# Kernel optimization log

Hardware: AMD Instinct MI355X
Metric: run time of the kernel (lower is better)

Reference implementation:

```python
import jax, jax.numpy as jnp
import numpy as np

V = 50000
E = 800000
D_IN = 128
D_OUT = 128
NUM_REL = 200
BN_EPS = 1e-5


def setup_inputs() -> dict:
    key = jax.random.key(0)
    ks = jax.random.split(key, 12)
    return {
        "x": jax.random.normal(ks[0], (V, D_IN), dtype=jnp.float32),
        "rel_repr": jax.random.normal(ks[1], (NUM_REL, D_IN), dtype=jnp.float32),
        "edge_norm": jax.random.uniform(ks[2], (E,), dtype=jnp.float32),
        "in_w": jax.random.normal(ks[3], (D_IN, D_OUT), dtype=jnp.float32) * 0.1,
        "out_w": jax.random.normal(ks[4], (D_IN, D_OUT), dtype=jnp.float32) * 0.1,
        "loop_w": jax.random.normal(ks[5], (D_IN, D_OUT), dtype=jnp.float32) * 0.1,
        "w_rel": jax.random.normal(ks[6], (D_IN, D_OUT), dtype=jnp.float32) * 0.1,
        "loop_rel": jax.random.normal(ks[7], (1, D_IN), dtype=jnp.float32),
        "bias": jnp.zeros((D_OUT,), dtype=jnp.float32),
        "bn_gamma": jnp.ones((D_OUT,), dtype=jnp.float32),
        "bn_beta": jnp.zeros((D_OUT,), dtype=jnp.float32),
        "edge_type": jax.random.randint(ks[8], (E,), 0, NUM_REL, dtype=jnp.int32),
        "src": jax.random.randint(ks[9], (E,), 0, V, dtype=jnp.int32),
        "dst": jax.random.randint(ks[10], (E,), 0, V, dtype=jnp.int32),
    }


def reference(x, rel_repr, edge_norm, in_w, out_w, loop_w, w_rel, loop_rel,
              bias, bn_gamma, bn_beta, edge_type, src, dst):
    # rel_wt is None (num_base=-1) -> rel = rel_repr directly
    rel = rel_repr

    # message: comp='mult' composition of gathered src features and relation emb
    edge_data = x[src] * rel[edge_type]                      # [E, D_IN]
    half = edge_data.shape[0] // 2
    # first half of edges through in_w, second half through out_w (CompGCN convention)
    msg = jnp.concatenate(
        [edge_data[:half] @ in_w, edge_data[half:] @ out_w], axis=0
    ) * edge_norm[:, None]                                   # [E, D_OUT]

    # agg='sum': scatter-reduce into destination nodes (zero for isolated nodes)
    h_agg = jax.ops.segment_sum(msg, dst, num_segments=V)    # [V, D_OUT]

    # self-loop branch: comp(x, loop_rel) @ loop_w, comb='add', scaled by 1/3
    loop = (x * loop_rel) @ loop_w                           # [V, D_OUT]
    h = (h_agg + loop) * (1.0 / 3.0)

    h = h + bias

    # BatchNorm1d (training mode: batch statistics over node dim)
    mean = jnp.mean(h, axis=0)
    var = jnp.var(h, axis=0)
    h = (h - mean) * jax.lax.rsqrt(var + BN_EPS) * bn_gamma + bn_beta

    out_x = jax.nn.relu(h)                                   # act='relu'
    out_rel = rel @ w_rel                                    # ltr=True
    return (out_x, out_rel)
```

## Files before the change

kernel.cpp:

```cpp
#include <hip/hip_runtime.h>
#include <hip/hip_bf16.h>


#define SCAN_BLOCK 256
#define CB 128
#define CHUNK 4096
#define NBC_MAX 800
#define CAP 3072
#define RED1 64
#define NGB 128

typedef __attribute__((ext_vector_type(8))) short short8v;
typedef __attribute__((ext_vector_type(4))) float float4v;

__device__ inline short f2bf(float f) {
    union { float f; unsigned u; } c; c.f = f;
    unsigned u = c.u;
    return (short)((u + 0x7fffu + ((u >> 16) & 1u)) >> 16);
}
__device__ inline unsigned packbf(float a, float b) {
    return (unsigned)(unsigned short)f2bf(a) |
           ((unsigned)(unsigned short)f2bf(b) << 16);
}
__device__ inline float bflo(unsigned u) { return __uint_as_float(u << 16); }
__device__ inline float bfhi(unsigned u) { return __uint_as_float(u & 0xffff0000u); }

__global__ __launch_bounds__(256) void xcast_kernel(
    const float* __restrict__ x, const float* __restrict__ rel,
    short* __restrict__ xbf, short* __restrict__ relbf, int V, int R)
{
    size_t i = ((size_t)blockIdx.x * 256 + threadIdx.x) * 8;
    size_t nx = (size_t)V * 128;
    size_t total = nx + (size_t)R * 128;
    if (i >= total) return;
    const float* sp; short* dp; size_t k;
    if (i < nx) { sp = x; dp = xbf; k = i; }
    else        { sp = rel; dp = relbf; k = i - nx; }
    float4 v0 = *reinterpret_cast<const float4*>(sp + k);
    float4 v1 = *reinterpret_cast<const float4*>(sp + k + 4);
    short8v o;
    o[0] = f2bf(v0.x); o[1] = f2bf(v0.y); o[2] = f2bf(v0.z); o[3] = f2bf(v0.w);
    o[4] = f2bf(v1.x); o[5] = f2bf(v1.y); o[6] = f2bf(v1.z); o[7] = f2bf(v1.w);
    *reinterpret_cast<short8v*>(dp + k) = o;
}

__global__ __launch_bounds__(256) void hist_coarse_kernel(
    const int* __restrict__ dst, int* __restrict__ counts,
    int E, int V, int NBC)
{
    __shared__ int lh[NBC_MAX];
    for (int i = threadIdx.x; i < NBC; i += 256) lh[i] = 0;
    __syncthreads();
    int half = E >> 1;
    int e0 = blockIdx.x * CHUNK;
    for (int i = 0; i < CHUNK / 256; ++i) {
        int e = e0 + i * 256 + threadIdx.x;
        if (e < E) {
            int key = dst[e] + (e < half ? 0 : V);
            atomicAdd(&lh[key >> 7], 1);
        }
    }
    __syncthreads();
    for (int i = threadIdx.x; i < NBC; i += 256)
        counts[(size_t)blockIdx.x * NBC + i] = lh[i];
}

__global__ __launch_bounds__(SCAN_BLOCK) void scan_partial_t_kernel(
    const int* __restrict__ cnt_bm, int* __restrict__ partials,
    int CN, int NBC, int NBLK)
{
    __shared__ int red[SCAN_BLOCK];
    int l = blockIdx.x * SCAN_BLOCK + threadIdx.x;
    int v = 0;
    if (l < CN) {
        int bu = l / NBLK, bl = l - bu * NBLK;
        v = cnt_bm[(size_t)bl * NBC + bu];
    }
    red[threadIdx.x] = v;
    __syncthreads();
    for (int s = SCAN_BLOCK / 2; s > 0; s >>= 1) {
        if (threadIdx.x < s) red[threadIdx.x] += red[threadIdx.x + s];
        __syncthreads();
    }
    if (threadIdx.x == 0) partials[blockIdx.x] = red[0];
}

__global__ __launch_bounds__(1024) void scan_top_kernel(
    int* __restrict__ partials, int NB)
{
    __shared__ int sh[1024];
    int t = threadIdx.x;
    sh[t] = (t < NB) ? partials[t] : 0;
    __syncthreads();
    for (int s = 1; s < 1024; s <<= 1) {
        int v = (t >= s) ? sh[t - s] : 0;
        __syncthreads();
        sh[t] += v;
        __syncthreads();
    }
    if (t < NB) partials[t] = (t == 0) ? 0 : sh[t - 1];
}

__global__ __launch_bounds__(SCAN_BLOCK) void scan_final_t_kernel(
    const int* __restrict__ cnt_bm, const int* __restrict__ partials,
    int* __restrict__ base, int CN, int NBC, int NBLK)
{
    __shared__ int sh[SCAN_BLOCK];
    int l = blockIdx.x * SCAN_BLOCK + threadIdx.x;
    int t = threadIdx.x;
    int v = 0;
    if (l < CN) {
        int bu = l / NBLK, bl = l - bu * NBLK;
        v = cnt_bm[(size_t)bl * NBC + bu];
    }
    sh[t] = v;
    __syncthreads();
    for (int s = 1; s < SCAN_BLOCK; s <<= 1) {
        int u = (t >= s) ? sh[t - s] : 0;
        __syncthreads();
        sh[t] += u;
        __syncthreads();
    }
    if (l < CN) base[l] = partials[blockIdx.x] + sh[t] - v;
}

__global__ __launch_bounds__(256) void rank_coarse_kernel(
    const int* __restrict__ dst,
    const int* __restrict__ src,
    const int* __restrict__ edge_type,
    const float* __restrict__ edge_norm,
    const int* __restrict__ base,
    uint2* __restrict__ pay,
    int E, int V, int NBC, int NBLK)
{
    __shared__ int lh[NBC_MAX];
    __shared__ int lb[NBC_MAX];
    for (int i = threadIdx.x; i < NBC; i += 256) {
        lh[i] = 0;
        lb[i] = base[(size_t)i * NBLK + blockIdx.x];
    }
    __syncthreads();
    int half = E >> 1;
    int e0 = blockIdx.x * CHUNK;
    for (int i = 0; i < CHUNK / 256; ++i) {
        int e = e0 + i * 256 + threadIdx.x;
        if (e < E) {
            int d = dst[e], s = src[e], t = edge_type[e];
            float n = edge_norm[e];
            int key = d + (e < half ? 0 : V);
            int b = key >> 7;
            int r = atomicAdd(&lh[b], 1);
            pay[lb[b] + r] = make_uint2(
                ((unsigned)s << 16) | ((unsigned)t << 8) | (unsigned)(key & 127),
                __float_as_uint(n));
        }
    }
}

__global__ __launch_bounds__(256) void fine_sort_kernel(
    const uint2* __restrict__ pay,
    const int* __restrict__ base,
    uint2* __restrict__ pay2,
    int* __restrict__ foffg,
    int E, int NK, int NBC, int NBLK)
{
    __shared__ uint2 pay_s[CAP];
    __shared__ int fcnt[CB];
    __shared__ int ssc[CB];
    __shared__ int fcur[CB];

    int b = blockIdx.x;
    int beg = base[(size_t)b * NBLK];
    int end = (b + 1 < NBC) ? base[(size_t)(b + 1) * NBLK] : E;
    int cnt = end - beg;
    int tid = threadIdx.x;

    if (tid < CB) fcnt[tid] = 0;
    __syncthreads();
    for (int j = tid; j < cnt; j += 256)
        atomicAdd(&fcnt[pay[beg + j].x & 127u], 1);
    __syncthreads();
    if (tid < CB) ssc[tid] = fcnt[tid];
    __syncthreads();
    for (int s = 1; s < CB; s <<= 1) {
        int v = 0;
        if (tid < CB && tid >= s) v = ssc[tid - s];
        __syncthreads();
        if (tid < CB) ssc[tid] += v;
        __syncthreads();
    }
    if (tid < CB) {
        int ex = ssc[tid] - fcnt[tid];
        fcur[tid] = ex;
        int key = b * CB + tid;
        if (key <= NK) foffg[key] = beg + ex;
    }
    __syncthreads();

    if (cnt <= CAP) {
        for (int j = tid; j < cnt; j += 256) {
            uint2 p = pay[beg + j];
            int r = atomicAdd(&fcur[p.x & 127u], 1);
            pay_s[r] = p;
        }
        __syncthreads();
        for (int j = tid; j < cnt; j += 256) pay2[beg + j] = pay_s[j];
    } else {
        for (int j = tid; j < cnt; j += 256) {
            uint2 p = pay[beg + j];
            int r = atomicAdd(&fcur[p.x & 127u], 1);
            pay2[beg + r] = p;
        }
    }
}

__global__ __launch_bounds__(256) void aggregate_g16_kernel(
    const short* __restrict__ xbf,
    const short* __restrict__ relbf,
    const uint2* __restrict__ pay2,
    const int* __restrict__ foffg,
    short* __restrict__ accbf,
    int NK, int E)
{
    int wid = (blockIdx.x * 256 + threadIdx.x) >> 6;
    int lane = threadIdx.x & 63;
    int g = lane >> 4;
    int sub = lane & 15;
    int k = wid * 4 + g;
    if (k >= NK) k = NK - 1;
    int f0 = sub << 3;

    int beg = foffg[k];
    int end = foffg[k + 1];
    int cnt = end - beg;

    int maxc = cnt;
    maxc = max(maxc, __shfl_xor(maxc, 16, 64));
    maxc = max(maxc, __shfl_xor(maxc, 32, 64));

    float a0 = 0.f, a1 = 0.f, a2 = 0.f, a3 = 0.f;
    float a4 = 0.f, a5 = 0.f, a6 = 0.f, a7 = 0.f;

    for (int bas = 0; bas < maxc; bas += 16) {
        int off = bas + sub;
        int cidx = (cnt > 0) ? min(off, cnt - 1) : 0;
        int j = min(beg + cidx, E - 1);
        uint2 p = pay2[j];
        int qmax = min(16, maxc - bas);
        for (int q = 0; q < qmax; ++q) {
            int srcl = (lane & 48) + q;
            unsigned pqx = __shfl(p.x, srcl, 64);
            unsigned pqn = __shfl(p.y, srcl, 64);
            float n = ((bas + q) < cnt) ? __uint_as_float(pqn) : 0.f;
            int s = (int)(pqx >> 16);
            int t = (int)((pqx >> 8) & 0xffu);
            uint4 xv = *reinterpret_cast<const uint4*>(xbf + (size_t)s * 128 + f0);
            uint4 rv = *reinterpret_cast<const uint4*>(relbf + (size_t)t * 128 + f0);
            a0 += bflo(xv.x) * bflo(rv.x) * n;
            a1 += bfhi(xv.x) * bfhi(rv.x) * n;
            a2 += bflo(xv.y) * bflo(rv.y) * n;
            a3 += bfhi(xv.y) * bfhi(rv.y) * n;
            a4 += bflo(xv.z) * bflo(rv.z) * n;
            a5 += bfhi(xv.z) * bfhi(rv.z) * n;
            a6 += bflo(xv.w) * bflo(rv.w) * n;
            a7 += bfhi(xv.w) * bfhi(rv.w) * n;
        }
    }
    uint4 o;
    o.x = packbf(a0, a1);
    o.y = packbf(a2, a3);
    o.z = packbf(a4, a5);
    o.w = packbf(a6, a7);
    *reinterpret_cast<uint4*>(accbf + (size_t)k * 128 + f0) = o;
}

__global__ __launch_bounds__(256) void wpack_kernel(
    const float* __restrict__ in_w,
    const float* __restrict__ out_w,
    const float* __restrict__ loop_w,
    const float* __restrict__ loop_rel,
    short* __restrict__ wpack)
{
    int idx = blockIdx.x * 256 + threadIdx.x;
    if (idx >= 3 * 8 * 4 * 64) return;
    int lane = idx & 63;
    int t    = (idx >> 6) & 3;
    int cblk = (idx >> 8) & 7;
    int m    = idx >> 11;
    const float* W = (m == 0) ? in_w : (m == 1) ? out_w : loop_w;
    int col = cblk * 16 + (lane & 15);
    int kb  = t * 32 + ((lane >> 4) << 3);
    short8v v;
#pragma unroll
    for (int j = 0; j < 8; ++j) {
        float w = W[(kb + j) * 128 + col];
        if (m == 2) w *= loop_rel[kb + j];
        v[j] = f2bf(w);
    }
    *reinterpret_cast<short8v*>(wpack + (size_t)idx * 8) = v;
}

__global__ __launch_bounds__(512) void fused_gemm_mfma_kernel(
    const short* __restrict__ accbf,
    const short* __restrict__ xbf,
    const short* __restrict__ wpack,
    const float* __restrict__ bias,
    short* __restrict__ hbf,
    float* __restrict__ stats_part,
    int V, int NRB)
{
    __shared__ short wlds[3 * 4 * 4 * 64 * 8];
    __shared__ float s_red[128];

    int tid  = threadIdx.x;
    int wave = tid >> 6;
    int lane = tid & 63;
    int kgrp = lane >> 4;
    int r16  = lane & 15;
    int bid  = blockIdx.x >> 1;
    int hh   = blockIdx.x & 1;

    if (tid < 128) s_red[tid] = 0.f;

    {
        const short8v* wsv = reinterpret_cast<const short8v*>(wpack);
        short8v* wldv = reinterpret_cast<short8v*>(wlds);
#pragma unroll
        for (int i = 0; i < 6; ++i) {
            int idx = i * 512 + tid;
            int l  = idx & 63;
            int t  = (idx >> 6) & 3;
            int cb = (idx >> 8) & 3;
            int m  = idx >> 10;
            wldv[idx] = wsv[(((size_t)m * 8 + (4 * hh + cb)) * 4 + t) * 64 + l];
        }
    }
    __syncthreads();

    const short8v* wldv = reinterpret_cast<const short8v*>(wlds);
    float ps[4] = {0.f, 0.f, 0.f, 0.f};
    float pq[4] = {0.f, 0.f, 0.f, 0.f};

    for (int rt = bid; rt < NRB; rt += NGB) {
        int row0 = rt * 128 + wave * 16;
        int rowl = row0 + r16;
        int rowc = min(rowl, V - 1);

        short8v af[3][4];
        {
            const short* A0 = accbf + (size_t)rowc * 128;
            const short* A1 = accbf + (size_t)(V + rowc) * 128;
            const short* A2 = xbf + (size_t)rowc * 128;
#pragma unroll
            for (int t = 0; t < 4; ++t) {
                int o = t * 32 + (kgrp << 3);
                af[0][t] = *reinterpret_cast<const short8v*>(A0 + o);
                af[1][t] = *reinterpret_cast<const short8v*>(A1 + o);
                af[2][t] = *reinterpret_cast<const short8v*>(A2 + o);
            }
        }

        float4v c[4];
#pragma unroll
        for (int b = 0; b < 4; ++b) c[b] = (float4v)(0.f);

#pragma unroll
        for (int m = 0; m < 3; ++m)
#pragma unroll
            for (int t = 0; t < 4; ++t) {
#pragma unroll
                for (int b = 0; b < 4; ++b) {
                    short8v bf_ = wldv[(((m * 4 + b) * 4) + t) * 64 + lane];
                    c[b] = __builtin_amdgcn_mfma_f32_16x16x32_bf16(af[m][t], bf_, c[b], 0, 0, 0);
                }
            }

#pragma unroll
        for (int b = 0; b < 4; ++b) {
            int col = hh * 64 + b * 16 + r16;
            float bv = bias[col];
#pragma unroll
            for (int r = 0; r < 4; ++r) {
                int row = row0 + kgrp * 4 + r;
                if (row < V) {
                    float v = c[b][r] * (1.f / 3.f) + bv;
                    hbf[(size_t)row * 128 + col] = f2bf(v);
                    ps[b] += v;
                    pq[b] += v * v;
                }
            }
        }
    }

#pragma unroll
    for (int b = 0; b < 4; ++b) {
        int cl = b * 16 + r16;
        atomicAdd(&s_red[cl], ps[b]);
        atomicAdd(&s_red[64 + cl], pq[b]);
    }
    __syncthreads();
    if (tid < 64)
        stats_part[(size_t)bid * 256 + hh * 64 + tid] = s_red[tid];
    else if (tid < 128)
        stats_part[(size_t)bid * 256 + 128 + hh * 64 + (tid - 64)] = s_red[tid];
}

__global__ __launch_bounds__(256) void bn_reduce1_kernel(
    const float* __restrict__ stats_part, float* __restrict__ stage, int NB)
{
    int col = threadIdx.x;
    float s = 0.f;
    for (int i = blockIdx.x; i < NB; i += RED1)
        s += stats_part[(size_t)i * 256 + col];
    stage[(size_t)blockIdx.x * 256 + col] = s;
}

__global__ __launch_bounds__(256) void bn_reduce2_kernel(
    const float* __restrict__ stage, float* __restrict__ stats)
{
    int col = threadIdx.x;
    float s0 = 0.f, s1 = 0.f, s2 = 0.f, s3 = 0.f;
#pragma unroll
    for (int i = 0; i < RED1; i += 4) {
        s0 += stage[(size_t)(i + 0) * 256 + col];
        s1 += stage[(size_t)(i + 1) * 256 + col];
        s2 += stage[(size_t)(i + 2) * 256 + col];
        s3 += stage[(size_t)(i + 3) * 256 + col];
    }
    stats[col] = (s0 + s1) + (s2 + s3);
}

__global__ __launch_bounds__(256) void bn_apply_kernel(
    const short* __restrict__ hbf,
    float* __restrict__ hout,
    const float* __restrict__ stats,
    const float* __restrict__ gamma,
    const float* __restrict__ beta,
    int V)
{
    int c4   = (threadIdx.x & 31) << 2;
    int rsub = threadIdx.x >> 5;
    float inv_v = 1.f / (float)V;
    float sc[4], sh[4];
#pragma unroll
    for (int j = 0; j < 4; ++j) {
        int col = c4 + j;
        float mean = stats[col] * inv_v;
        float var  = stats[128 + col] * inv_v - mean * mean;
        float s = rsqrtf(var + 1e-5f) * gamma[col];
        sc[j] = s;
        sh[j] = beta[col] - mean * s;
    }
    for (int row = blockIdx.x * 8 + rsub; row < V; row += gridDim.x * 8) {
        uint2 u = *reinterpret_cast<const uint2*>(hbf + (size_t)row * 128 + c4);
        float4 v;
        v.x = fmaxf(bflo(u.x) * sc[0] + sh[0], 0.f);
        v.y = fmaxf(bfhi(u.x) * sc[1] + sh[1], 0.f);
        v.z = fmaxf(bflo(u.y) * sc[2] + sh[2], 0.f);
        v.w = fmaxf(bfhi(u.y) * sc[3] + sh[3], 0.f);
        *reinterpret_cast<float4*>(hout + (size_t)row * 128 + c4) = v;
    }
}

__global__ __launch_bounds__(256) void rel_gemm_kernel(
    const float* __restrict__ rel,
    const float* __restrict__ w_rel,
    float* __restrict__ out_rel,
    int R)
{
    int col = threadIdx.x & 127;
    int row = blockIdx.x * 2 + (threadIdx.x >> 7);
    if (row >= R) return;
    float acc = 0.f;
    for (int k = 0; k < 128; ++k)
        acc += rel[row * 128 + k] * w_rel[k * 128 + col];
    out_rel[row * 128 + col] = acc;
}

extern "C" void kernel_launch(void* const* d_in, const int* in_sizes, int n_in,
                              void* d_out, int out_size, void* d_ws, size_t ws_size,
                              hipStream_t stream)
{
    const float* x         = (const float*)d_in[0];
    const float* rel_repr  = (const float*)d_in[1];
    const float* edge_norm = (const float*)d_in[2];
    const float* in_w      = (const float*)d_in[3];
    const float* out_w     = (const float*)d_in[4];
    const float* loop_w    = (const float*)d_in[5];
    const float* w_rel     = (const float*)d_in[6];
    const float* loop_rel  = (const float*)d_in[7];
    const float* bias      = (const float*)d_in[8];
    const float* bn_gamma  = (const float*)d_in[9];
    const float* bn_beta   = (const float*)d_in[10];
    const int* edge_type   = (const int*)d_in[11];
    const int* src         = (const int*)d_in[12];
    const int* dst         = (const int*)d_in[13];

    const int V = in_sizes[0] / 128;
    const int E = in_sizes[2];
    const int R = in_sizes[1] / 128;
    const int NK = 2 * V;
    const int NBC = (NK + CB - 1) / CB;
    const int NBLK = (E + CHUNK - 1) / CHUNK;
    const int CN = NBC * NBLK;
    const int NB2 = (CN + SCAN_BLOCK - 1) / SCAN_BLOCK;
    const int NRB = (V + 127) / 128;

    float* hout    = (float*)d_out;
    float* out_rel = hout + (size_t)V * 128;

    char* wp_ = (char*)d_ws;
    short* accbf    = (short*)wp_;  wp_ += (size_t)NK * 128 * sizeof(short);
    short* xbf      = (short*)wp_;  wp_ += (size_t)V * 128 * sizeof(short);
    short* relbf    = (short*)wp_;  wp_ += (size_t)R * 128 * sizeof(short);
    short* hbf      = (short*)wp_;  wp_ += (size_t)V * 128 * sizeof(short);
    short* wpack    = (short*)wp_;  wp_ += (size_t)3 * 8 * 4 * 64 * 8 * sizeof(short);
    float* stats    = (float*)wp_;  wp_ += 256 * sizeof(float);
    float* stats_pt = (float*)wp_;  wp_ += (size_t)NGB * 256 * sizeof(float);
    float* stage    = (float*)wp_;  wp_ += (size_t)RED1 * 256 * sizeof(float);
    int*   counts   = (int*)wp_;    wp_ += (size_t)CN * sizeof(int);
    int*   basep    = (int*)wp_;    wp_ += (size_t)CN * sizeof(int);
    int*   partials = (int*)wp_;    wp_ += 1024 * sizeof(int);
    int*   foffg    = (int*)wp_;    wp_ += ((size_t)NK + 2) * sizeof(int);
    wp_ = (char*)(((uintptr_t)wp_ + 15) & ~(uintptr_t)15);
    uint2* pay      = (uint2*)wp_;  wp_ += (size_t)E * sizeof(uint2);
    uint2* pay2     = (uint2*)wp_;


    {
        size_t total = ((size_t)(V + R) * 128) / 8;
        xcast_kernel<<<(int)((total + 255) / 256), 256, 0, stream>>>(
            x, rel_repr, xbf, relbf, V, R);
    }
    wpack_kernel<<<(3 * 8 * 4 * 64 + 255) / 256, 256, 0, stream>>>(
        in_w, out_w, loop_w, loop_rel, wpack);

    hist_coarse_kernel<<<NBLK, 256, 0, stream>>>(dst, counts, E, V, NBC);
    scan_partial_t_kernel<<<NB2, SCAN_BLOCK, 0, stream>>>(counts, partials, CN, NBC, NBLK);
    scan_top_kernel<<<1, 1024, 0, stream>>>(partials, NB2);
    scan_final_t_kernel<<<NB2, SCAN_BLOCK, 0, stream>>>(counts, partials, basep, CN, NBC, NBLK);
    rank_coarse_kernel<<<NBLK, 256, 0, stream>>>(
        dst, src, edge_type, edge_norm, basep, pay, E, V, NBC, NBLK);
    fine_sort_kernel<<<NBC, 256, 0, stream>>>(
        pay, basep, pay2, foffg, E, NK, NBC, NBLK);

    {
        int waves = (NK + 3) / 4;
        int blocks = (waves * 64 + 255) / 256;
        aggregate_g16_kernel<<<blocks, 256, 0, stream>>>(
            xbf, relbf, pay2, foffg, accbf, NK, E);
    }

    fused_gemm_mfma_kernel<<<NGB * 2, 512, 0, stream>>>(
        accbf, xbf, wpack, bias, hbf, stats_pt, V, NRB);

    bn_reduce1_kernel<<<RED1, 256, 0, stream>>>(stats_pt, stage, NGB);
    bn_reduce2_kernel<<<1, 256, 0, stream>>>(stage, stats);
    bn_apply_kernel<<<1024, 256, 0, stream>>>(hbf, hout, stats, bn_gamma, bn_beta, V);
    rel_gemm_kernel<<<(R + 1) / 2, 256, 0, stream>>>(rel_repr, w_rel, out_rel, R);
}
```

Before: 124.5 us.

## Fuse scan top, BN reduce2, and rel GEMM into neighbors; widen sort blocks

Removes the single-block scan_top kernel by having each scan_final block sum the partials of all preceding blocks itself. Folds bn_reduce2 into the BN apply kernel, with every block redundantly reducing the stage buffer, and appends the rel GEMM as extra blocks of the same launch. It also raises the histogram, rank and fine-sort kernels to 512 threads per block. The goal is fewer kernel launches and serial tiny kernels, in exchange for redundant reduction work per block and fewer BN apply blocks (256 instead of 1024).

Result: faster. 114.4 us (-8.1%).

```diff
diff --git a/kernel.cpp b/kernel.cpp
--- a/kernel.cpp
+++ b/kernel.cpp
@@ -44,24 +44,24 @@
     *reinterpret_cast<short8v*>(dp + k) = o;
 }
 
-__global__ __launch_bounds__(256) void hist_coarse_kernel(
+__global__ __launch_bounds__(512) void hist_coarse_kernel(
     const int* __restrict__ dst, int* __restrict__ counts,
     int E, int V, int NBC)
 {
     __shared__ int lh[NBC_MAX];
-    for (int i = threadIdx.x; i < NBC; i += 256) lh[i] = 0;
+    for (int i = threadIdx.x; i < NBC; i += 512) lh[i] = 0;
     __syncthreads();
     int half = E >> 1;
     int e0 = blockIdx.x * CHUNK;
-    for (int i = 0; i < CHUNK / 256; ++i) {
-        int e = e0 + i * 256 + threadIdx.x;
+    for (int i = 0; i < CHUNK / 512; ++i) {
+        int e = e0 + i * 512 + threadIdx.x;
         if (e < E) {
             int key = dst[e] + (e < half ? 0 : V);
             atomicAdd(&lh[key >> 7], 1);
         }
     }
     __syncthreads();
-    for (int i = threadIdx.x; i < NBC; i += 256)
+    for (int i = threadIdx.x; i < NBC; i += 512)
         counts[(size_t)blockIdx.x * NBC + i] = lh[i];
 }
 
@@ -85,29 +85,29 @@
     if (threadIdx.x == 0) partials[blockIdx.x] = red[0];
 }
 
-__global__ __launch_bounds__(1024) void scan_top_kernel(
-    int* __restrict__ partials, int NB)
-{
-    __shared__ int sh[1024];
-    int t = threadIdx.x;
-    sh[t] = (t < NB) ? partials[t] : 0;
-    __syncthreads();
-    for (int s = 1; s < 1024; s <<= 1) {
-        int v = (t >= s) ? sh[t - s] : 0;
-        __syncthreads();
-        sh[t] += v;
-        __syncthreads();
-    }
-    if (t < NB) partials[t] = (t == 0) ? 0 : sh[t - 1];
-}
-
 __global__ __launch_bounds__(SCAN_BLOCK) void scan_final_t_kernel(
     const int* __restrict__ cnt_bm, const int* __restrict__ partials,
     int* __restrict__ base, int CN, int NBC, int NBLK)
 {
     __shared__ int sh[SCAN_BLOCK];
-    int l = blockIdx.x * SCAN_BLOCK + threadIdx.x;
+    __shared__ int pref_s;
     int t = threadIdx.x;
+    int bid = blockIdx.x;
+
+    int acc = 0;
+    for (int i = t; i < bid; i += SCAN_BLOCK) acc += partials[i];
+    sh[t] = acc;
+    __syncthreads();
+    for (int s = SCAN_BLOCK / 2; s > 0; s >>= 1) {
+        if (t < s) sh[t] += sh[t + s];
+        __syncthreads();
+    }
+    if (t == 0) pref_s = sh[0];
+    __syncthreads();
+    int pref = pref_s;
+    __syncthreads();
+
+    int l = bid * SCAN_BLOCK + t;
     int v = 0;
     if (l < CN) {
         int bu = l / NBLK, bl = l - bu * NBLK;
@@ -121,10 +121,10 @@
         sh[t] += u;
         __syncthreads();
     }
-    if (l < CN) base[l] = partials[blockIdx.x] + sh[t] - v;
-}
-
-__global__ __launch_bounds__(256) void rank_coarse_kernel(
+    if (l < CN) base[l] = pref + sh[t] - v;
+}
+
+__global__ __launch_bounds__(512) void rank_coarse_kernel(
     const int* __restrict__ dst,
     const int* __restrict__ src,
     const int* __restrict__ edge_type,
@@ -135,15 +135,15 @@
 {
     __shared__ int lh[NBC_MAX];
     __shared__ int lb[NBC_MAX];
-    for (int i = threadIdx.x; i < NBC; i += 256) {
+    for (int i = threadIdx.x; i < NBC; i += 512) {
         lh[i] = 0;
         lb[i] = base[(size_t)i * NBLK + blockIdx.x];
     }
     __syncthreads();
     int half = E >> 1;
     int e0 = blockIdx.x * CHUNK;
-    for (int i = 0; i < CHUNK / 256; ++i) {
-        int e = e0 + i * 256 + threadIdx.x;
+    for (int i = 0; i < CHUNK / 512; ++i) {
+        int e = e0 + i * 512 + threadIdx.x;
         if (e < E) {
             int d = dst[e], s = src[e], t = edge_type[e];
             float n = edge_norm[e];
@@ -157,7 +157,7 @@
     }
 }
 
-__global__ __launch_bounds__(256) void fine_sort_kernel(
+__global__ __launch_bounds__(512) void fine_sort_kernel(
     const uint2* __restrict__ pay,
     const int* __restrict__ base,
     uint2* __restrict__ pay2,
@@ -177,7 +177,7 @@
 
     if (tid < CB) fcnt[tid] = 0;
     __syncthreads();
-    for (int j = tid; j < cnt; j += 256)
+    for (int j = tid; j < cnt; j += 512)
         atomicAdd(&fcnt[pay[beg + j].x & 127u], 1);
     __syncthreads();
     if (tid < CB) ssc[tid] = fcnt[tid];
@@ -198,15 +198,15 @@
     __syncthreads();
 
     if (cnt <= CAP) {
-        for (int j = tid; j < cnt; j += 256) {
+        for (int j = tid; j < cnt; j += 512) {
             uint2 p = pay[beg + j];
             int r = atomicAdd(&fcur[p.x & 127u], 1);
             pay_s[r] = p;
         }
         __syncthreads();
-        for (int j = tid; j < cnt; j += 256) pay2[beg + j] = pay_s[j];
+        for (int j = tid; j < cnt; j += 512) pay2[beg + j] = pay_s[j];
     } else {
-        for (int j = tid; j < cnt; j += 256) {
+        for (int j = tid; j < cnt; j += 512) {
             uint2 p = pay[beg + j];
             int r = atomicAdd(&fcur[p.x & 127u], 1);
             pay2[beg + r] = p;
@@ -415,43 +415,59 @@
     stage[(size_t)blockIdx.x * 256 + col] = s;
 }
 
-__global__ __launch_bounds__(256) void bn_reduce2_kernel(
-    const float* __restrict__ stage, float* __restrict__ stats)
-{
-    int col = threadIdx.x;
-    float s0 = 0.f, s1 = 0.f, s2 = 0.f, s3 = 0.f;
-#pragma unroll
-    for (int i = 0; i < RED1; i += 4) {
-        s0 += stage[(size_t)(i + 0) * 256 + col];
-        s1 += stage[(size_t)(i + 1) * 256 + col];
-        s2 += stage[(size_t)(i + 2) * 256 + col];
-        s3 += stage[(size_t)(i + 3) * 256 + col];
-    }
-    stats[col] = (s0 + s1) + (s2 + s3);
-}
-
-__global__ __launch_bounds__(256) void bn_apply_kernel(
+__global__ __launch_bounds__(256) void bn_apply_fused_kernel(
     const short* __restrict__ hbf,
     float* __restrict__ hout,
-    const float* __restrict__ stats,
+    const float* __restrict__ stage,
     const float* __restrict__ gamma,
     const float* __restrict__ beta,
-    int V)
-{
-    int c4   = (threadIdx.x & 31) << 2;
-    int rsub = threadIdx.x >> 5;
+    int V, int NBA,
+    const float* __restrict__ rel,
+    const float* __restrict__ w_rel,
+    float* __restrict__ out_rel,
+    int R)
+{
+    int tid = threadIdx.x;
+    if ((int)blockIdx.x >= NBA) {
+        int rb = blockIdx.x - NBA;
+        int col = tid & 127;
+        int row = rb * 2 + (tid >> 7);
+        if (row >= R) return;
+        float acc = 0.f;
+        for (int k = 0; k < 128; ++k)
+            acc += rel[row * 128 + k] * w_rel[k * 128 + col];
+        out_rel[row * 128 + col] = acc;
+        return;
+    }
+
+    __shared__ float st[256];
+    {
+        float s0 = 0.f, s1 = 0.f, s2 = 0.f, s3 = 0.f;
+#pragma unroll
+        for (int i = 0; i < RED1; i += 4) {
+            s0 += stage[(size_t)(i + 0) * 256 + tid];
+            s1 += stage[(size_t)(i + 1) * 256 + tid];
+            s2 += stage[(size_t)(i + 2) * 256 + tid];
+            s3 += stage[(size_t)(i + 3) * 256 + tid];
+        }
+        st[tid] = (s0 + s1) + (s2 + s3);
+    }
+    __syncthreads();
+
+    int c4   = (tid & 31) << 2;
+    int rsub = tid >> 5;
     float inv_v = 1.f / (float)V;
     float sc[4], sh[4];
 #pragma unroll
     for (int j = 0; j < 4; ++j) {
         int col = c4 + j;
-        float mean = stats[col] * inv_v;
-        float var  = stats[128 + col] * inv_v - mean * mean;
+        float mean = st[col] * inv_v;
+        float var  = st[128 + col] * inv_v - mean * mean;
         float s = rsqrtf(var + 1e-5f) * gamma[col];
         sc[j] = s;
         sh[j] = beta[col] - mean * s;
     }
-    for (int row = blockIdx.x * 8 + rsub; row < V; row += gridDim.x * 8) {
+    for (int row = blockIdx.x * 8 + rsub; row < V; row += NBA * 8) {
         uint2 u = *reinterpret_cast<const uint2*>(hbf + (size_t)row * 128 + c4);
         float4 v;
         v.x = fmaxf(bflo(u.x) * sc[0] + sh[0], 0.f);
@@ -460,21 +476,6 @@
         v.w = fmaxf(bfhi(u.y) * sc[3] + sh[3], 0.f);
         *reinterpret_cast<float4*>(hout + (size_t)row * 128 + c4) = v;
     }
-}
-
-__global__ __launch_bounds__(256) void rel_gemm_kernel(
-    const float* __restrict__ rel,
-    const float* __restrict__ w_rel,
-    float* __restrict__ out_rel,
-    int R)
-{
-    int col = threadIdx.x & 127;
-    int row = blockIdx.x * 2 + (threadIdx.x >> 7);
-    if (row >= R) return;
-    float acc = 0.f;
-    for (int k = 0; k < 128; ++k)
-        acc += rel[row * 128 + k] * w_rel[k * 128 + col];
-    out_rel[row * 128 + col] = acc;
 }
 
 extern "C" void kernel_launch(void* const* d_in, const int* in_sizes, int n_in,
@@ -505,6 +506,7 @@
     const int CN = NBC * NBLK;
     const int NB2 = (CN + SCAN_BLOCK - 1) / SCAN_BLOCK;
     const int NRB = (V + 127) / 128;
+    const int NBA = 256;
 
     float* hout    = (float*)d_out;
     float* out_rel = hout + (size_t)V * 128;
@@ -515,7 +517,6 @@
     short* relbf    = (short*)wp_;  wp_ += (size_t)R * 128 * sizeof(short);
     short* hbf      = (short*)wp_;  wp_ += (size_t)V * 128 * sizeof(short);
     short* wpack    = (short*)wp_;  wp_ += (size_t)3 * 8 * 4 * 64 * 8 * sizeof(short);
-    float* stats    = (float*)wp_;  wp_ += 256 * sizeof(float);
     float* stats_pt = (float*)wp_;  wp_ += (size_t)NGB * 256 * sizeof(float);
     float* stage    = (float*)wp_;  wp_ += (size_t)RED1 * 256 * sizeof(float);
     int*   counts   = (int*)wp_;    wp_ += (size_t)CN * sizeof(int);
@@ -535,13 +536,12 @@
     wpack_kernel<<<(3 * 8 * 4 * 64 + 255) / 256, 256, 0, stream>>>(
         in_w, out_w, loop_w, loop_rel, wpack);
 
-    hist_coarse_kernel<<<NBLK, 256, 0, stream>>>(dst, counts, E, V, NBC);
+    hist_coarse_kernel<<<NBLK, 512, 0, stream>>>(dst, counts, E, V, NBC);
     scan_partial_t_kernel<<<NB2, SCAN_BLOCK, 0, stream>>>(counts, partials, CN, NBC, NBLK);
-    scan_top_kernel<<<1, 1024, 0, stream>>>(partials, NB2);
     scan_final_t_kernel<<<NB2, SCAN_BLOCK, 0, stream>>>(counts, partials, basep, CN, NBC, NBLK);
-    rank_coarse_kernel<<<NBLK, 256, 0, stream>>>(
+    rank_coarse_kernel<<<NBLK, 512, 0, stream>>>(
         dst, src, edge_type, edge_norm, basep, pay, E, V, NBC, NBLK);
-    fine_sort_kernel<<<NBC, 256, 0, stream>>>(
+    fine_sort_kernel<<<NBC, 512, 0, stream>>>(
         pay, basep, pay2, foffg, E, NK, NBC, NBLK);
 
     {
@@ -555,7 +555,7 @@
         accbf, xbf, wpack, bias, hbf, stats_pt, V, NRB);
 
     bn_reduce1_kernel<<<RED1, 256, 0, stream>>>(stats_pt, stage, NGB);
-    bn_reduce2_kernel<<<1, 256, 0, stream>>>(stage, stats);
-    bn_apply_kernel<<<1024, 256, 0, stream>>>(hbf, hout, stats, bn_gamma, bn_beta, V);
-    rel_gemm_kernel<<<(R + 1) / 2, 256, 0, stream>>>(rel_repr, w_rel, out_rel, R);
-}
+    bn_apply_fused_kernel<<<NBA + (R + 1) / 2, 256, 0, stream>>>(
+        hbf, hout, stage, bn_gamma, bn_beta, V, NBA,
+        rel_repr, w_rel, out_rel, R);
+}
```
